# Optimization experiments

Measured on AMD Instinct MI355X. Metric: run time of the kernel, lower is better.

## Reference

```python
import jax, jax.numpy as jnp
import numpy as np

D_MODEL = 768
D_INNER = 1536      # expand*d_model
D_STATE = 128
NHEADS = 12         # d_inner // headdim
HEADDIM = 128
D_CONV = 4
CONV_DIM = D_INNER + 2 * D_STATE   # 1792 (ngroups=1)
D_IN_PROJ = 2 * D_INNER + 2 * D_STATE + NHEADS  # 3340


def setup_inputs() -> dict:
    key = jax.random.key(0)
    it = iter(jax.random.split(key, 24))
    def rn(shape, s):
        return jax.random.normal(next(it), shape, jnp.float32) * s
    inp = {}
    inp['x'] = jax.random.normal(next(it), (8, 12, 4096), jnp.float32)
    # conv stem
    inp['w1'] = rn((192, 12, 5), 0.2); inp['b1'] = jnp.zeros((192,))
    inp['bn1_g'] = jnp.ones((192,)); inp['bn1_b'] = jnp.zeros((192,)); inp['bn1_m'] = jnp.zeros((192,)); inp['bn1_v'] = jnp.ones((192,))
    inp['w2'] = rn((384, 192, 3), 0.05); inp['b2'] = jnp.zeros((384,))
    inp['bn2_g'] = jnp.ones((384,)); inp['bn2_b'] = jnp.zeros((384,)); inp['bn2_m'] = jnp.zeros((384,)); inp['bn2_v'] = jnp.ones((384,))
    inp['w3'] = rn((768, 384, 3), 0.05); inp['b3'] = jnp.zeros((768,))
    inp['bn3_g'] = jnp.ones((768,)); inp['bn3_b'] = jnp.zeros((768,)); inp['bn3_m'] = jnp.zeros((768,)); inp['bn3_v'] = jnp.ones((768,))
    # Mamba2 backbone
    inp['in_proj_w'] = rn((D_IN_PROJ, D_MODEL), 0.02)
    inp['conv_w'] = rn((CONV_DIM, D_CONV), 0.2)
    inp['conv_b'] = jnp.zeros((CONV_DIM,))
    inp['dt_bias'] = rn((NHEADS,), 0.5)
    inp['A_log'] = jnp.log(jax.random.uniform(next(it), (NHEADS,), minval=1.0, maxval=16.0))
    inp['D'] = jnp.ones((NHEADS,))
    inp['norm_w'] = jnp.ones((D_INNER,))
    inp['out_proj_w'] = rn((D_MODEL, D_INNER), 0.02)
    # classifier
    inp['fc1_w'] = rn((1024, 768), 0.02); inp['fc1_b'] = jnp.zeros((1024,))
    inp['bnc_g'] = jnp.ones((1024,)); inp['bnc_b'] = jnp.zeros((1024,)); inp['bnc_m'] = jnp.zeros((1024,)); inp['bnc_v'] = jnp.ones((1024,))
    inp['fc2_w'] = rn((27, 1024), 0.02); inp['fc2_b'] = jnp.zeros((27,))
    return inp


def _conv1d(x, w, b, stride, pad):
    y = jax.lax.conv_general_dilated(x, w, (stride,), [(pad, pad)], dimension_numbers=('NCH', 'OIH', 'NCH'))
    return y + b[None, :, None]


def _bn(x, g, b, m, v, eps=1e-5):
    sh = (1, -1, 1) if x.ndim == 3 else (1, -1)
    return (x - m.reshape(sh)) * jax.lax.rsqrt(v.reshape(sh) + eps) * g.reshape(sh) + b.reshape(sh)


def _forward(x, w1, b1, bn1_g, bn1_b, bn1_m, bn1_v, w2, b2, bn2_g, bn2_b, bn2_m, bn2_v,
             w3, b3, bn3_g, bn3_b, bn3_m, bn3_v, in_proj_w, conv_w, conv_b, dt_bias,
             A_log, D, norm_w, out_proj_w, fc1_w, fc1_b, bnc_g, bnc_b, bnc_m, bnc_v, fc2_w, fc2_b):
    gelu = lambda t: jax.nn.gelu(t, approximate=False)
    # conv stem (B, 12, 4096) -> (B, 768, 1024)
    h = _bn(gelu(_conv1d(x, w1, b1, 2, 2)), bn1_g, bn1_b, bn1_m, bn1_v)
    h = _bn(gelu(_conv1d(h, w2, b2, 2, 1)), bn2_g, bn2_b, bn2_m, bn2_v)
    h = _bn(gelu(_conv1d(h, w3, b3, 1, 1)), bn3_g, bn3_b, bn3_m, bn3_v)
    u = h.transpose(0, 2, 1)  # (B, L, 768)
    # Mamba2
    zxbcdt = u @ in_proj_w.T  # (B, L, 3340)
    z = zxbcdt[..., :D_INNER]
    xBC = zxbcdt[..., D_INNER:D_INNER + CONV_DIM]
    dt = jax.nn.softplus(zxbcdt[..., D_INNER + CONV_DIM:] + dt_bias)  # (B, L, H)
    # causal depthwise conv over time + silu
    xc = jax.lax.conv_general_dilated(xBC.transpose(0, 2, 1), conv_w[:, None, :], (1,), [(D_CONV - 1, 0)],
                                      dimension_numbers=('NCH', 'OIH', 'NCH'), feature_group_count=CONV_DIM)
    xBC = jax.nn.silu(xc + conv_b[None, :, None]).transpose(0, 2, 1)
    xs = xBC[..., :D_INNER]
    Bm = xBC[..., D_INNER:D_INNER + D_STATE]   # (B, L, N), ngroups=1
    Cm = xBC[..., D_INNER + D_STATE:]
    A = -jnp.exp(A_log)  # (H,)
    b_, l_ = xs.shape[0], xs.shape[1]
    xh = xs.reshape(b_, l_, NHEADS, HEADDIM)
    dA = jnp.exp(dt * A)  # (B, L, H)
    tm = lambda t: jnp.moveaxis(t, 1, 0)
    def step(state, inps):
        x_t, dA_t, dt_t, B_t, C_t = inps
        # state: (B, H, P, N)
        state = state * dA_t[..., None, None] + (dt_t[..., None] * x_t)[..., None] * B_t[:, None, None, :]
        y_t = jnp.einsum('bhpn,bn->bhp', state, C_t)
        return state, y_t
    state0 = jnp.zeros((b_, NHEADS, HEADDIM, D_STATE), xs.dtype)
    _, ys = jax.lax.scan(step, state0, (tm(xh), tm(dA), tm(dt), tm(Bm), tm(Cm)))
    y = jnp.moveaxis(ys, 0, 1) + D[None, None, :, None] * xh  # (B, L, H, P)
    y = y.reshape(b_, l_, D_INNER)
    # gated RMSNorm (norm_before_gate=False)
    y = y * jax.nn.silu(z)
    y = y * jax.lax.rsqrt(jnp.mean(y * y, axis=-1, keepdims=True) + 1e-5) * norm_w
    out = y @ out_proj_w.T  # (B, L, 768)
    rep = out.mean(axis=1)
    h1 = jax.nn.relu(_bn(rep @ fc1_w.T + fc1_b, bnc_g, bnc_b, bnc_m, bnc_v))
    return h1 @ fc2_w.T + fc2_b


def reference(x, w1, b1, bn1_g, bn1_b, bn1_m, bn1_v, w2, b2, bn2_g, bn2_b, bn2_m, bn2_v,
              w3, b3, bn3_g, bn3_b, bn3_m, bn3_v, in_proj_w, conv_w, conv_b, dt_bias,
              A_log, D, norm_w, out_proj_w, fc1_w, fc1_b, bnc_g, bnc_b, bnc_m, bnc_v, fc2_w, fc2_b):
    return _forward(x, w1, b1, bn1_g, bn1_b, bn1_m, bn1_v, w2, b2, bn2_g, bn2_b, bn2_m, bn2_v,
                    w3, b3, bn3_g, bn3_b, bn3_m, bn3_v, in_proj_w, conv_w, conv_b, dt_bias,
                    A_log, D, norm_w, out_proj_w, fc1_w, fc1_b, bnc_g, bnc_b, bnc_m, bnc_v, fc2_w, fc2_b)
```

## Files before the change

### kernel.cpp

```cpp
#include <hip/hip_runtime.h>
#include <math.h>

#define DEV __device__ __forceinline__

DEV float geluf(float x){ return 0.5f*x*(1.0f+erff(x*0.7071067811865476f)); }
DEV float siluf(float x){ return x/(1.0f+expf(-x)); }
DEV float softplusf(float x){ return fmaxf(x,0.0f)+log1pf(expf(-fabsf(x))); }
DEV unsigned short f2bf(float f){
  unsigned int u = __float_as_uint(f);
  unsigned int r = (u + 0x7fffu + ((u>>16)&1u)) >> 16;
  return (unsigned short)r;
}

typedef __attribute__((ext_vector_type(8))) short short8;
typedef __attribute__((ext_vector_type(4))) float f32x4;

__global__ void conv1_k(const float* __restrict__ x, const float* __restrict__ w,
                        const float* __restrict__ bias,
                        const float* __restrict__ g, const float* __restrict__ bb,
                        const float* __restrict__ m, const float* __restrict__ v,
                        float* __restrict__ out){
  int t  = blockIdx.x*256 + threadIdx.x;
  int og = blockIdx.y;
  int b  = blockIdx.z;
  const float* xb = x + (size_t)b*12*4096;
  float acc[8];
  #pragma unroll
  for(int oo=0;oo<8;++oo) acc[oo] = bias[og*8+oo];
  for(int i=0;i<12;++i){
    float xv[5];
    #pragma unroll
    for(int k=0;k<5;++k){
      int src = 2*t + k - 2;
      xv[k] = (src>=0 && src<4096) ? xb[i*4096+src] : 0.0f;
    }
    #pragma unroll
    for(int oo=0;oo<8;++oo){
      const float* wr = w + (size_t)(og*8+oo)*60 + i*5;
      #pragma unroll
      for(int k=0;k<5;++k) acc[oo] = fmaf(wr[k], xv[k], acc[oo]);
    }
  }
  #pragma unroll
  for(int oo=0;oo<8;++oo){
    int o = og*8+oo;
    float y = geluf(acc[oo]);
    float sc = g[o]*rsqrtf(v[o]+1e-5f);
    y = (y-m[o])*sc + bb[o];
    out[(size_t)b*192*2048 + (size_t)o*2048 + t] = y;
  }
}

__global__ void xpose1_k(const float* __restrict__ h1, unsigned short* __restrict__ T1){
  __shared__ float tile[32][33];
  int t0 = blockIdx.x*32, i0 = blockIdx.y*32, b = blockIdx.z;
  int c = threadIdx.x & 31, r4 = threadIdx.x >> 5;
  const float* src = h1 + (size_t)b*393216;
  #pragma unroll
  for(int i=0;i<4;++i){ int r = r4 + i*8; tile[r][c] = src[(size_t)(i0+r)*2048 + t0 + c]; }
  __syncthreads();
  unsigned short* dst = T1 + (size_t)b*2048*192;
  #pragma unroll
  for(int i=0;i<4;++i){ int r = r4 + i*8;
    dst[(size_t)(t0+r)*192 + i0 + c] = f2bf(tile[c][r]);
  }
}

__global__ void wprep_k(const float* __restrict__ ipw, const float* __restrict__ w2,
                        const float* __restrict__ w3, unsigned short* __restrict__ Wb,
                        unsigned short* __restrict__ w2r, unsigned short* __restrict__ w3r){
  int gid = blockIdx.x*256 + threadIdx.x;
  if(gid < 2555904){
    Wb[gid] = f2bf(ipw[gid]);
  } else if(gid < 2555904+221184){
    int g2 = gid - 2555904;
    int o = g2 / 576, rem = g2 - o*576, k = rem / 192, i = rem - k*192;
    w2r[g2] = f2bf(w2[(size_t)o*576 + i*3 + k]);
  } else if(gid < 2555904+221184+884736){
    int g3 = gid - 2555904 - 221184;
    int o = g3 / 1152, rem = g3 - o*1152, k = rem / 384, i = rem - k*384;
    w3r[g3] = f2bf(w3[(size_t)o*1152 + i*3 + k]);
  }
}

__global__ __launch_bounds__(256) void conv2_mfma(const unsigned short* __restrict__ A,
                                                  const unsigned short* __restrict__ W,
                                                  const float* __restrict__ bias,
                                                  const float* __restrict__ g, const float* __restrict__ bb,
                                                  const float* __restrict__ bm, const float* __restrict__ bv,
                                                  unsigned short* __restrict__ outb){
  __shared__ unsigned short As[4096], Bs[4096];
  const int tid = threadIdx.x;
  const int lane = tid & 63, wave = tid >> 6;
  const int wm = wave & 1, wn = wave >> 1;
  const int m0 = blockIdx.y*128, n0 = blockIdx.x*128;
  const int bidx = m0 >> 10, tloc = m0 & 1023;
  f32x4 acc[4][4];
  #pragma unroll
  for(int i=0;i<4;++i)
    #pragma unroll
    for(int j=0;j<4;++j) acc[i][j] = (f32x4){0.f,0.f,0.f,0.f};
  const int u0 = tid, u1 = tid + 256;
  const int r0 = u0>>2, kl0 = (u0&3) ^ ((r0>>1)&3);
  const int r1 = u1>>2, kl1 = (u1&3) ^ ((r1>>1)&3);
  const int kg = lane>>4, ml = lane&15;
  const short8 z8 = {0,0,0,0,0,0,0,0};
  for(int kb=0; kb<3; ++kb){
    int ta = 2*(tloc + r0) + kb - 1;
    int tb = 2*(tloc + r1) + kb - 1;
    bool va = (ta>=0) && (ta<2048);
    bool vb = (tb>=0) && (tb<2048);
    const unsigned short* pa = A + ((size_t)bidx*2048 + ta)*192;
    const unsigned short* pb = A + ((size_t)bidx*2048 + tb)*192;
    for(int c0=0; c0<192; c0+=32){
      int k0 = kb*192 + c0;
      short8 a0 = va ? *reinterpret_cast<const short8*>(pa + c0 + kl0*8) : z8;
      short8 a1 = vb ? *reinterpret_cast<const short8*>(pb + c0 + kl1*8) : z8;
      short8 b0 = *reinterpret_cast<const short8*>(W + (size_t)(n0+r0)*576 + k0 + kl0*8);
      short8 b1 = *reinterpret_cast<const short8*>(W + (size_t)(n0+r1)*576 + k0 + kl1*8);
      __syncthreads();
      *reinterpret_cast<short8*>(As + u0*8) = a0;
      *reinterpret_cast<short8*>(As + u1*8) = a1;
      *reinterpret_cast<short8*>(Bs + u0*8) = b0;
      *reinterpret_cast<short8*>(Bs + u1*8) = b1;
      __syncthreads();
      short8 af[4], bfr[4];
      #pragma unroll
      for(int f=0;f<4;++f){
        int row = wm*64 + f*16 + ml;
        int un  = row*4 + (kg ^ ((row>>1)&3));
        af[f] = *reinterpret_cast<const short8*>(As + un*8);
        int rowb = wn*64 + f*16 + ml;
        int ub   = rowb*4 + (kg ^ ((rowb>>1)&3));
        bfr[f] = *reinterpret_cast<const short8*>(Bs + ub*8);
      }
      #pragma unroll
      for(int i=0;i<4;++i)
        #pragma unroll
        for(int j=0;j<4;++j)
          acc[i][j] = __builtin_amdgcn_mfma_f32_16x16x32_bf16(af[i], bfr[j], acc[i][j], 0, 0, 0);
    }
  }
  #pragma unroll
  for(int i=0;i<4;++i){
    int rb = m0 + wm*64 + i*16 + kg*4;
    #pragma unroll
    for(int j=0;j<4;++j){
      int col = n0 + wn*64 + j*16 + ml;
      float sc = g[col]*rsqrtf(bv[col]+1e-5f);
      float mm = bm[col], bbv = bb[col], bi = bias[col];
      #pragma unroll
      for(int r=0;r<4;++r){
        float yv = geluf(acc[i][j][r] + bi);
        yv = (yv - mm)*sc + bbv;
        outb[(size_t)(rb+r)*384 + col] = f2bf(yv);
      }
    }
  }
}

__global__ __launch_bounds__(256) void conv3_mfma(const unsigned short* __restrict__ A,
                                                  const unsigned short* __restrict__ W,
                                                  const float* __restrict__ bias,
                                                  const float* __restrict__ g, const float* __restrict__ bb,
                                                  const float* __restrict__ bm, const float* __restrict__ bv,
                                                  unsigned short* __restrict__ outb,
                                                  float* __restrict__ outf){
  __shared__ unsigned short As[4096], Bs[4096];
  const int tid = threadIdx.x;
  const int lane = tid & 63, wave = tid >> 6;
  const int wm = wave & 1, wn = wave >> 1;
  const int m0 = blockIdx.y*128, n0 = blockIdx.x*128;
  const int bidx = m0 >> 10, tloc = m0 & 1023;
  f32x4 acc[4][4];
  #pragma unroll
  for(int i=0;i<4;++i)
    #pragma unroll
    for(int j=0;j<4;++j) acc[i][j] = (f32x4){0.f,0.f,0.f,0.f};
  const int u0 = tid, u1 = tid + 256;
  const int r0 = u0>>2, kl0 = (u0&3) ^ ((r0>>1)&3);
  const int r1 = u1>>2, kl1 = (u1&3) ^ ((r1>>1)&3);
  const int kg = lane>>4, ml = lane&15;
  const short8 z8 = {0,0,0,0,0,0,0,0};
  for(int kb=0; kb<3; ++kb){
    int ta = tloc + r0 + kb - 1;
    int tb = tloc + r1 + kb - 1;
    bool va = (ta>=0) && (ta<1024);
    bool vb = (tb>=0) && (tb<1024);
    const unsigned short* pa = A + ((size_t)bidx*1024 + ta)*384;
    const unsigned short* pb = A + ((size_t)bidx*1024 + tb)*384;
    for(int c0=0; c0<384; c0+=32){
      int k0 = kb*384 + c0;
      short8 a0 = va ? *reinterpret_cast<const short8*>(pa + c0 + kl0*8) : z8;
      short8 a1 = vb ? *reinterpret_cast<const short8*>(pb + c0 + kl1*8) : z8;
      short8 b0 = *reinterpret_cast<const short8*>(W + (size_t)(n0+r0)*1152 + k0 + kl0*8);
      short8 b1 = *reinterpret_cast<const short8*>(W + (size_t)(n0+r1)*1152 + k0 + kl1*8);
      __syncthreads();
      *reinterpret_cast<short8*>(As + u0*8) = a0;
      *reinterpret_cast<short8*>(As + u1*8) = a1;
      *reinterpret_cast<short8*>(Bs + u0*8) = b0;
      *reinterpret_cast<short8*>(Bs + u1*8) = b1;
      __syncthreads();
      short8 af[4], bfr[4];
      #pragma unroll
      for(int f=0;f<4;++f){
        int row = wm*64 + f*16 + ml;
        int un  = row*4 + (kg ^ ((row>>1)&3));
        af[f] = *reinterpret_cast<const short8*>(As + un*8);
        int rowb = wn*64 + f*16 + ml;
        int ub   = rowb*4 + (kg ^ ((rowb>>1)&3));
        bfr[f] = *reinterpret_cast<const short8*>(Bs + ub*8);
      }
      #pragma unroll
      for(int i=0;i<4;++i)
        #pragma unroll
        for(int j=0;j<4;++j)
          acc[i][j] = __builtin_amdgcn_mfma_f32_16x16x32_bf16(af[i], bfr[j], acc[i][j], 0, 0, 0);
    }
  }
  #pragma unroll
  for(int i=0;i<4;++i){
    int rb = m0 + wm*64 + i*16 + kg*4;
    #pragma unroll
    for(int j=0;j<4;++j){
      int col = n0 + wn*64 + j*16 + ml;
      float sc = g[col]*rsqrtf(bv[col]+1e-5f);
      float mm = bm[col], bbv = bb[col], bi = bias[col];
      #pragma unroll
      for(int r=0;r<4;++r){
        float yv = geluf(acc[i][j][r] + bi);
        yv = (yv - mm)*sc + bbv;
        outb[(size_t)(rb+r)*768 + col] = f2bf(yv);
        outf[(size_t)(rb+r)*768 + col] = yv;
      }
    }
  }
}

__global__ __launch_bounds__(256) void inproj_mfma(const unsigned short* __restrict__ A,
                                                   const unsigned short* __restrict__ B,
                                                   float* __restrict__ Z, float* __restrict__ XB){
  __shared__ unsigned short As[4096], Bs[4096];
  const int tid = threadIdx.x;
  const int lane = tid & 63, wave = tid >> 6;
  const int wm = wave & 1, wn = wave >> 1;
  const int m0 = blockIdx.y*128, n0 = blockIdx.x*128;
  f32x4 acc[4][4];
  #pragma unroll
  for(int i=0;i<4;++i)
    #pragma unroll
    for(int j=0;j<4;++j) acc[i][j] = (f32x4){0.f,0.f,0.f,0.f};
  const int u0 = tid, u1 = tid + 256;
  const int r0 = u0>>2, kl0 = (u0&3) ^ ((r0>>1)&3);
  const int r1 = u1>>2, kl1 = (u1&3) ^ ((r1>>1)&3);
  const int kg = lane>>4, ml = lane&15;
  for(int k0=0;k0<768;k0+=32){
    short8 a0 = *reinterpret_cast<const short8*>(A + (size_t)(m0+r0)*768 + k0 + kl0*8);
    short8 a1 = *reinterpret_cast<const short8*>(A + (size_t)(m0+r1)*768 + k0 + kl1*8);
    short8 b0 = *reinterpret_cast<const short8*>(B + (size_t)(n0+r0)*768 + k0 + kl0*8);
    short8 b1 = *reinterpret_cast<const short8*>(B + (size_t)(n0+r1)*768 + k0 + kl1*8);
    __syncthreads();
    *reinterpret_cast<short8*>(As + u0*8) = a0;
    *reinterpret_cast<short8*>(As + u1*8) = a1;
    *reinterpret_cast<short8*>(Bs + u0*8) = b0;
    *reinterpret_cast<short8*>(Bs + u1*8) = b1;
    __syncthreads();
    short8 af[4], bfr[4];
    #pragma unroll
    for(int f=0;f<4;++f){
      int row = wm*64 + f*16 + ml;
      int un  = row*4 + (kg ^ ((row>>1)&3));
      af[f] = *reinterpret_cast<const short8*>(As + un*8);
      int rowb = wn*64 + f*16 + ml;
      int ub   = rowb*4 + (kg ^ ((rowb>>1)&3));
      bfr[f] = *reinterpret_cast<const short8*>(Bs + ub*8);
    }
    #pragma unroll
    for(int i=0;i<4;++i)
      #pragma unroll
      for(int j=0;j<4;++j)
        acc[i][j] = __builtin_amdgcn_mfma_f32_16x16x32_bf16(af[i], bfr[j], acc[i][j], 0, 0, 0);
  }
  float* op; int cb; int stride;
  if(n0 < 1536){ op = Z;  cb = n0;        stride = 1536; }
  else         { op = XB; cb = n0 - 1536; stride = 1792; }
  #pragma unroll
  for(int i=0;i<4;++i){
    int rb = m0 + wm*64 + i*16 + kg*4;
    #pragma unroll
    for(int j=0;j<4;++j){
      int col = cb + wn*64 + j*16 + ml;
      #pragma unroll
      for(int r=0;r<4;++r)
        op[(size_t)(rb+r)*stride + col] = acc[i][j][r];
    }
  }
}

__global__ __launch_bounds__(256) void dtgemm2_k(const float* __restrict__ h3f, const float* __restrict__ W,
                                                 const float* __restrict__ dt_bias, const float* __restrict__ A_log,
                                                 float* __restrict__ dt, float* __restrict__ dA){
  __shared__ float Ws[12][768];
  __shared__ float Ah[12], Bh[12];
  int tid = threadIdx.x;
  for(int idx=tid; idx<9216; idx+=256){
    int hh = idx/768, k = idx - hh*768;
    Ws[hh][k] = W[(size_t)(3328+hh)*768 + k];
  }
  if(tid<12){ Ah[tid] = -expf(A_log[tid]); Bh[tid] = dt_bias[tid]; }
  __syncthreads();
  int wave = tid>>6, lane = tid&63;
  int m = blockIdx.x*4 + wave;
  const float* xr = h3f + (size_t)m*768;
  float xv[12];
  #pragma unroll
  for(int q=0;q<12;++q) xv[q] = xr[q*64+lane];
  float res[12];
  #pragma unroll
  for(int h=0;h<12;++h){
    float acc = 0.f;
    #pragma unroll
    for(int q=0;q<12;++q) acc = fmaf(xv[q], Ws[h][q*64+lane], acc);
    #pragma unroll
    for(int off=32;off;off>>=1) acc += __shfl_xor(acc, off);
    res[h] = acc;
  }
  if(lane==0){
    #pragma unroll
    for(int h=0;h<12;++h){
      float sp = softplusf(res[h] + Bh[h]);
      dt[(size_t)m*12+h] = sp;
      dA[(size_t)m*12+h] = expf(sp*Ah[h]);
    }
  }
}

__global__ void dwconv_k(const float* __restrict__ XB, const float* __restrict__ cw,
                         const float* __restrict__ cb, float* __restrict__ xs,
                         float* __restrict__ Bo, float* __restrict__ Co){
  int gid = blockIdx.x*256 + threadIdx.x;
  int c4 = gid % 448;
  int m = gid / 448;
  int t = m & 1023;
  int c = c4*4;
  float wA[4][4];
  #pragma unroll
  for(int i=0;i<4;++i)
    *reinterpret_cast<float4*>(wA[i]) = *reinterpret_cast<const float4*>(&cw[(c+i)*4]);
  float4 bi = *reinterpret_cast<const float4*>(&cb[c]);
  float av[4] = {bi.x, bi.y, bi.z, bi.w};
  #pragma unroll
  for(int j=0;j<4;++j){
    int tt = t - 3 + j;
    if(tt >= 0){
      float4 xv = *reinterpret_cast<const float4*>(&XB[(size_t)(m-3+j)*1792 + c]);
      av[0] = fmaf(wA[0][j], xv.x, av[0]);
      av[1] = fmaf(wA[1][j], xv.y, av[1]);
      av[2] = fmaf(wA[2][j], xv.z, av[2]);
      av[3] = fmaf(wA[3][j], xv.w, av[3]);
    }
  }
  float4 res = make_float4(siluf(av[0]), siluf(av[1]), siluf(av[2]), siluf(av[3]));
  if(c4 < 384)      *reinterpret_cast<float4*>(&xs[(size_t)m*1536 + c])        = res;
  else if(c4 < 416) *reinterpret_cast<float4*>(&Bo[(size_t)m*128 + (c-1536)])  = res;
  else              *reinterpret_cast<float4*>(&Co[(size_t)m*128 + (c-1664)])  = res;
}

__global__ void cumda_k(const float* __restrict__ dA, float* __restrict__ cda){
  __shared__ float ld[1024];
  int bh = blockIdx.x; int b = bh/12, hh = bh - b*12;
  int tid = threadIdx.x;
  for(int i=tid;i<1024;i+=128) ld[i] = dA[((size_t)b*1024 + i)*12 + hh];
  __syncthreads();
  for(int c=0;c<8;++c){
    int base = c*128;
    for(int off=1;off<128;off<<=1){
      float v = ld[base+tid];
      if(tid>=off) v *= ld[base+tid-off];
      __syncthreads();
      ld[base+tid] = v;
      __syncthreads();
    }
  }
  for(int i=tid;i<1024;i+=128) cda[(size_t)bh*1024 + i] = ld[i];
}

#define SSTEP(E, BQE, CQE) \
  s[0][jj*4+E] = fmaf(s[0][jj*4+E], dav, c0*BQE); y0 = fmaf(s[0][jj*4+E], CQE, y0); \
  s[1][jj*4+E] = fmaf(s[1][jj*4+E], dav, c1*BQE); y1 = fmaf(s[1][jj*4+E], CQE, y1); \
  s[2][jj*4+E] = fmaf(s[2][jj*4+E], dav, c2*BQE); y2 = fmaf(s[2][jj*4+E], CQE, y2); \
  s[3][jj*4+E] = fmaf(s[3][jj*4+E], dav, c3*BQE); y3 = fmaf(s[3][jj*4+E], CQE, y3);

__global__ __launch_bounds__(128) void scan_chunk_k(float* __restrict__ xs,
    const float* __restrict__ Bm, const float* __restrict__ Cm,
    const float* __restrict__ dtb, const float* __restrict__ dAb,
    const float* __restrict__ Dv, float* __restrict__ sfin){
  const int c = blockIdx.x, h = blockIdx.y, b = blockIdx.z;
  const int tid = threadIdx.x;
  const int ng = tid & 3, pg = tid >> 2;
  __shared__ float lx[16][128], lB[16][144], lC[16][144], ly[16][128];
  __shared__ float ldt[16], lda_[16];
  float s[4][32];
  #pragma unroll
  for(int i=0;i<4;++i)
    #pragma unroll
    for(int j=0;j<32;++j) s[i][j]=0.f;
  const float Dh = Dv[h];
  const size_t mb = (size_t)b*1024 + (size_t)c*128;
  for(int t0=0;t0<128;t0+=16){
    for(int idx=tid; idx<2048; idx+=128){
      int tl = idx>>7, cc = idx&127;
      lx[tl][cc] = xs[(mb+t0+tl)*1536 + h*128 + cc];
      int slot = (cc>>5)*36 + (cc&31);
      lB[tl][slot] = Bm[(mb+t0+tl)*128 + cc];
      lC[tl][slot] = Cm[(mb+t0+tl)*128 + cc];
    }
    if(tid<16){
      ldt[tid]  = dtb[(mb+t0+tid)*12 + h];
      lda_[tid] = dAb[(mb+t0+tid)*12 + h];
    }
    __syncthreads();
    for(int tl=0; tl<16; ++tl){
      float dtv = ldt[tl], dav = lda_[tl];
      float4 xq = *reinterpret_cast<const float4*>(&lx[tl][pg*4]);
      float c0 = dtv*xq.x, c1 = dtv*xq.y, c2 = dtv*xq.z, c3 = dtv*xq.w;
      float y0=0.f,y1=0.f,y2=0.f,y3=0.f;
      #pragma unroll
      for(int jj=0;jj<8;++jj){
        float4 bq = *reinterpret_cast<const float4*>(&lB[tl][ng*36+jj*4]);
        float4 cq = *reinterpret_cast<const float4*>(&lC[tl][ng*36+jj*4]);
        SSTEP(0, bq.x, cq.x)
        SSTEP(1, bq.y, cq.y)
        SSTEP(2, bq.z, cq.z)
        SSTEP(3, bq.w, cq.w)
      }
      y0 += __shfl_xor(y0,1); y0 += __shfl_xor(y0,2);
      y1 += __shfl_xor(y1,1); y1 += __shfl_xor(y1,2);
      y2 += __shfl_xor(y2,1); y2 += __shfl_xor(y2,2);
      y3 += __shfl_xor(y3,1); y3 += __shfl_xor(y3,2);
      if(ng==0) *reinterpret_cast<float4*>(&ly[tl][pg*4]) = make_float4(y0,y1,y2,y3);
    }
    __syncthreads();
    for(int idx=tid; idx<2048; idx+=128){
      int tl = idx>>7, cc = idx&127;
      xs[(mb+t0+tl)*1536 + h*128 + cc] = ly[tl][cc] + Dh*lx[tl][cc];
    }
    __syncthreads();
  }
  float* dst = sfin + ((size_t)(b*12+h)*8 + c)*16384;
  #pragma unroll
  for(int jj=0;jj<8;++jj)
    #pragma unroll
    for(int e=0;e<4;++e){
      int n = ng*32 + jj*4 + e;
      *reinterpret_cast<float4*>(&dst[(size_t)n*128 + pg*4]) =
        make_float4(s[0][jj*4+e], s[1][jj*4+e], s[2][jj*4+e], s[3][jj*4+e]);
    }
}

__global__ __launch_bounds__(256) void correct_k(const float* __restrict__ Cm,
    const float* __restrict__ cumdA, const float* __restrict__ sfin,
    float* __restrict__ ys){
  const int c = blockIdx.x + 1, h = blockIdx.y, b = blockIdx.z;
  const int tid = threadIdx.x;
  const size_t bh = (size_t)b*12 + h;
  __shared__ float Sl[16][128];
  __shared__ float Cl[16][132];
  __shared__ float cumP[128];
  __shared__ float coefs[8];
  if(tid==0){
    float cf = 1.f;
    for(int cp=c-1; cp>=0; --cp){
      coefs[cp] = cf;
      cf *= cumdA[bh*1024 + (size_t)cp*128 + 127];
    }
  }
  if(tid<128) cumP[tid] = cumdA[bh*1024 + (size_t)c*128 + tid];
  __syncthreads();
  const int tp = tid>>4, tt = tid&15;
  float acc[8][8];
  #pragma unroll
  for(int i=0;i<8;++i)
    #pragma unroll
    for(int j=0;j<8;++j) acc[i][j]=0.f;
  const size_t mb = (size_t)b*1024 + (size_t)c*128;
  for(int n0=0;n0<128;n0+=16){
    {
      int kk = tid>>4, po = tid&15;
      float4 v0 = {0,0,0,0}, v1 = {0,0,0,0};
      for(int cp=0; cp<c; ++cp){
        const float* sp = sfin + ((bh*8 + cp)*16384) + (size_t)(n0+kk)*128 + po*8;
        float4 a0 = *reinterpret_cast<const float4*>(sp);
        float4 a1 = *reinterpret_cast<const float4*>(sp+4);
        float cf = coefs[cp];
        v0.x = fmaf(cf,a0.x,v0.x); v0.y = fmaf(cf,a0.y,v0.y);
        v0.z = fmaf(cf,a0.z,v0.z); v0.w = fmaf(cf,a0.w,v0.w);
        v1.x = fmaf(cf,a1.x,v1.x); v1.y = fmaf(cf,a1.y,v1.y);
        v1.z = fmaf(cf,a1.z,v1.z); v1.w = fmaf(cf,a1.w,v1.w);
      }
      *reinterpret_cast<float4*>(&Sl[kk][po*8])   = v0;
      *reinterpret_cast<float4*>(&Sl[kk][po*8+4]) = v1;
    }
    #pragma unroll
    for(int e=0;e<8;++e){
      int idx = tid*8 + e; int tl = idx>>4, kk = idx&15;
      Cl[kk][tl] = Cm[(mb + tl)*128 + n0 + kk];
    }
    __syncthreads();
    #pragma unroll
    for(int kk=0;kk<16;++kk){
      float4 sa = *reinterpret_cast<const float4*>(&Sl[kk][tp*8]);
      float4 sb = *reinterpret_cast<const float4*>(&Sl[kk][tp*8+4]);
      float4 ca = *reinterpret_cast<const float4*>(&Cl[kk][tt*8]);
      float4 cb = *reinterpret_cast<const float4*>(&Cl[kk][tt*8+4]);
      float sv[8] = {sa.x,sa.y,sa.z,sa.w,sb.x,sb.y,sb.z,sb.w};
      float cv[8] = {ca.x,ca.y,ca.z,ca.w,cb.x,cb.y,cb.z,cb.w};
      #pragma unroll
      for(int i=0;i<8;++i)
        #pragma unroll
        for(int j=0;j<8;++j) acc[i][j] = fmaf(sv[i], cv[j], acc[i][j]);
    }
    __syncthreads();
  }
  #pragma unroll
  for(int j=0;j<8;++j){
    int tl = tt*8 + j;
    float cp = cumP[tl];
    float* yp = ys + (mb + tl)*1536 + h*128 + tp*8;
    float4 y0 = *reinterpret_cast<float4*>(yp);
    float4 y1 = *reinterpret_cast<float4*>(yp+4);
    y0.x += cp*acc[0][j]; y0.y += cp*acc[1][j]; y0.z += cp*acc[2][j]; y0.w += cp*acc[3][j];
    y1.x += cp*acc[4][j]; y1.y += cp*acc[5][j]; y1.z += cp*acc[6][j]; y1.w += cp*acc[7][j];
    *reinterpret_cast<float4*>(yp)   = y0;
    *reinterpret_cast<float4*>(yp+4) = y1;
  }
}

__global__ void gate_k(const float* __restrict__ ys, const float* __restrict__ Z,
                       const float* __restrict__ nw, float* __restrict__ ybp){
  int m = blockIdx.x;
  int b = m >> 10, t = m & 1023;
  int tid = threadIdx.x;
  float gvals[6];
  float ss = 0.0f;
  #pragma unroll
  for(int r=0;r<6;++r){
    int c = r*256 + tid;
    float yv = ys[(size_t)m*1536 + c];
    float zv = Z[(size_t)m*1536 + c];
    float gv = yv * siluf(zv);
    gvals[r] = gv;
    ss = fmaf(gv, gv, ss);
  }
  #pragma unroll
  for(int off=32;off;off>>=1) ss += __shfl_xor(ss, off);
  __shared__ float red[4];
  if((tid&63)==0) red[tid>>6] = ss;
  __syncthreads();
  float tot = red[0]+red[1]+red[2]+red[3];
  float scale = rsqrtf(tot*(1.0f/1536.0f) + 1e-5f);
  float* dst = ybp + ((size_t)(t&7)*8 + b)*1536;
  #pragma unroll
  for(int r=0;r<6;++r){
    int c = r*256 + tid;
    atomicAdd(&dst[c], gvals[r]*scale*nw[c]);
  }
}

__global__ void ybm_k(const float* __restrict__ ybp, float* __restrict__ ybm){
  int idx = blockIdx.x*256 + threadIdx.x;
  float s = 0.0f;
  #pragma unroll
  for(int p=0;p<8;++p) s += ybp[(size_t)p*12288 + idx];
  ybm[idx] = s * (1.0f/1024.0f);
}

__global__ void rep_k(const float* __restrict__ ybm, const float* __restrict__ W,
                      float* __restrict__ rep){
  int wid  = (blockIdx.x<<2) + (threadIdx.x>>6);
  int lane = threadIdx.x & 63;
  int b = wid / 768, o = wid % 768;
  const float* xr = ybm + (size_t)b*1536;
  const float* wr = W + (size_t)o*1536;
  float acc = 0.0f;
  for(int c=lane;c<1536;c+=64) acc = fmaf(xr[c], wr[c], acc);
  #pragma unroll
  for(int off=32;off;off>>=1) acc += __shfl_xor(acc, off);
  if(lane==0) rep[wid] = acc;
}

__global__ void fc1_k(const float* __restrict__ rep, const float* __restrict__ W,
                      const float* __restrict__ bias, const float* __restrict__ g,
                      const float* __restrict__ bb, const float* __restrict__ m,
                      const float* __restrict__ v, float* __restrict__ out){
  int wid  = (blockIdx.x<<2) + (threadIdx.x>>6);
  int lane = threadIdx.x & 63;
  int b = wid >> 10, o = wid & 1023;
  const float* xr = rep + (size_t)b*768;
  const float* wr = W + (size_t)o*768;
  float acc = 0.0f;
  for(int c=lane;c<768;c+=64) acc = fmaf(xr[c], wr[c], acc);
  #pragma unroll
  for(int off=32;off;off>>=1) acc += __shfl_xor(acc, off);
  if(lane==0){
    float val = acc + bias[o];
    float sc = g[o]*rsqrtf(v[o]+1e-5f);
    val = (val - m[o])*sc + bb[o];
    out[wid] = fmaxf(val, 0.0f);
  }
}

__global__ void fc2_k(const float* __restrict__ h1, const float* __restrict__ W,
                      const float* __restrict__ bias, float* __restrict__ out){
  int wid  = (blockIdx.x<<2) + (threadIdx.x>>6);
  int lane = threadIdx.x & 63;
  int b = wid / 27, o = wid % 27;
  const float* xr = h1 + (size_t)b*1024;
  const float* wr = W + (size_t)o*1024;
  float acc = 0.0f;
  for(int c=lane;c<1024;c+=64) acc = fmaf(xr[c], wr[c], acc);
  #pragma unroll
  for(int off=32;off;off>>=1) acc += __shfl_xor(acc, off);
  if(lane==0) out[wid] = acc + bias[o];
}

#define OFF_H1     0u
#define OFF_T1     3145728u
#define OFF_T2     4718592u
#define OFF_H3T    6291456u
#define OFF_WB     9437184u
#define OFF_W2R    10715136u
#define OFF_W3R    10825728u
#define OFF_Z      12582912u
#define OFF_XB     25165824u
#define OFF_XS     39944192u
#define OFF_H3F    39944192u
#define OFF_B      52527104u
#define OFF_C      53575680u
#define OFF_DT     54624256u
#define OFF_DA     54722560u
#define OFF_SLOT98K 54820864u
#define OFF_YBM    54919168u
#define OFF_REP    54931456u
#define OFF_FC1    54937600u
#define OFF_SFIN   0u

extern "C" void kernel_launch(void* const* d_in, const int* in_sizes, int n_in,
                              void* d_out, int out_size, void* d_ws, size_t ws_size,
                              hipStream_t stream){
  const float* x       = (const float*)d_in[0];
  const float* w1      = (const float*)d_in[1];
  const float* b1      = (const float*)d_in[2];
  const float* bn1g    = (const float*)d_in[3];
  const float* bn1b    = (const float*)d_in[4];
  const float* bn1m    = (const float*)d_in[5];
  const float* bn1v    = (const float*)d_in[6];
  const float* w2      = (const float*)d_in[7];
  const float* b2      = (const float*)d_in[8];
  const float* bn2g    = (const float*)d_in[9];
  const float* bn2b    = (const float*)d_in[10];
  const float* bn2m    = (const float*)d_in[11];
  const float* bn2v    = (const float*)d_in[12];
  const float* w3      = (const float*)d_in[13];
  const float* b3      = (const float*)d_in[14];
  const float* bn3g    = (const float*)d_in[15];
  const float* bn3b    = (const float*)d_in[16];
  const float* bn3m    = (const float*)d_in[17];
  const float* bn3v    = (const float*)d_in[18];
  const float* ipw     = (const float*)d_in[19];
  const float* convw   = (const float*)d_in[20];
  const float* convb   = (const float*)d_in[21];
  const float* dtbias  = (const float*)d_in[22];
  const float* Alog    = (const float*)d_in[23];
  const float* Dvec    = (const float*)d_in[24];
  const float* normw   = (const float*)d_in[25];
  const float* opw     = (const float*)d_in[26];
  const float* fc1w    = (const float*)d_in[27];
  const float* fc1b    = (const float*)d_in[28];
  const float* bncg    = (const float*)d_in[29];
  const float* bncb    = (const float*)d_in[30];
  const float* bncm    = (const float*)d_in[31];
  const float* bncv    = (const float*)d_in[32];
  const float* fc2w    = (const float*)d_in[33];
  const float* fc2b    = (const float*)d_in[34];

  float* ws   = (float*)d_ws;
  float* h1   = ws + OFF_H1;
  unsigned short* T1  = (unsigned short*)(ws + OFF_T1);
  unsigned short* T2  = (unsigned short*)(ws + OFF_T2);
  unsigned short* h3t = (unsigned short*)(ws + OFF_H3T);
  unsigned short* Wb  = (unsigned short*)(ws + OFF_WB);
  unsigned short* w2r = (unsigned short*)(ws + OFF_W2R);
  unsigned short* w3r = (unsigned short*)(ws + OFF_W3R);
  float* Zb   = ws + OFF_Z;
  float* XBb  = ws + OFF_XB;
  float* xsb  = ws + OFF_XS;
  float* h3f  = ws + OFF_H3F;
  float* Bb   = ws + OFF_B;
  float* Cb   = ws + OFF_C;
  float* dtb  = ws + OFF_DT;
  float* dAb  = ws + OFF_DA;
  float* slot = ws + OFF_SLOT98K;
  float* ybm  = ws + OFF_YBM;
  float* rep  = ws + OFF_REP;
  float* f1b  = ws + OFF_FC1;
  float* sfin = ws + OFF_SFIN;
  float* outp = (float*)d_out;

  conv1_k<<<dim3(8,24,8),  256, 0, stream>>>(x, w1, b1, bn1g, bn1b, bn1m, bn1v, h1);
  xpose1_k<<<dim3(64,6,8), 256, 0, stream>>>(h1, T1);
  wprep_k<<<14304, 256, 0, stream>>>(ipw, w2, w3, Wb, w2r, w3r);
  conv2_mfma<<<dim3(3,64), 256, 0, stream>>>(T1, w2r, b2, bn2g, bn2b, bn2m, bn2v, T2);
  conv3_mfma<<<dim3(6,64), 256, 0, stream>>>(T2, w3r, b3, bn3g, bn3b, bn3m, bn3v, h3t, h3f);
  dtgemm2_k<<<2048, 256, 0, stream>>>(h3f, ipw, dtbias, Alog, dtb, dAb);
  inproj_mfma<<<dim3(26,64), 256, 0, stream>>>(h3t, Wb, Zb, XBb);
  dwconv_k<<<14336, 256, 0, stream>>>(XBb, convw, convb, xsb, Bb, Cb);
  cumda_k<<<96, 128, 0, stream>>>(dAb, slot);
  scan_chunk_k<<<dim3(8,12,8), 128, 0, stream>>>(xsb, Bb, Cb, dtb, dAb, Dvec, sfin);
  correct_k<<<dim3(7,12,8), 256, 0, stream>>>(Cb, slot, sfin, xsb);
  hipMemsetAsync(slot, 0, 98304*sizeof(float), stream);
  gate_k<<<8192, 256, 0, stream>>>(xsb, Zb, normw, slot);
  ybm_k<<<48, 256, 0, stream>>>(slot, ybm);
  rep_k<<<1536, 256, 0, stream>>>(ybm, opw, rep);
  fc1_k<<<2048, 256, 0, stream>>>(rep, fc1w, fc1b, bncg, bncb, bncm, bncv, f1b);
  fc2_k<<<54, 256, 0, stream>>>(f1b, fc2w, fc2b, outp);
}
```

Before: 751.1 us.

## Replace sequential intra-chunk scan with SSD matrix form on bf16 MFMA

The per-chunk sequential recurrence kernel is replaced by a chunked SSD formulation. Each chunk computes C·Bᵀ, applies a causal mask with exp(cumsum log-decay) weights, multiplies by dt·x, and forms the chunk-end state, all as bf16 MFMA matmuls in swizzled LDS. The cumulative decay is now a log-space prefix sum, and B/C are stored as bf16 to halve their traffic. The goal is to turn a latency-bound serial loop into matrix-core work. The cost is reduced precision from bf16 x/B/C, partly offset by a hi/lo split of the decay matrix.

```diff
diff --git a/kernel.cpp b/kernel.cpp
--- a/kernel.cpp
+++ b/kernel.cpp
@@ -11,6 +11,7 @@
   unsigned int r = (u + 0x7fffu + ((u>>16)&1u)) >> 16;
   return (unsigned short)r;
 }
+DEV float bf2f(unsigned short u){ return __uint_as_float(((unsigned int)u)<<16); }
 
 typedef __attribute__((ext_vector_type(8))) short short8;
 typedef __attribute__((ext_vector_type(4))) float f32x4;
@@ -298,16 +299,16 @@
 }
 
 __global__ __launch_bounds__(256) void dtgemm2_k(const float* __restrict__ h3f, const float* __restrict__ W,
-                                                 const float* __restrict__ dt_bias, const float* __restrict__ A_log,
-                                                 float* __restrict__ dt, float* __restrict__ dA){
+                                                 const float* __restrict__ dt_bias,
+                                                 float* __restrict__ dt){
   __shared__ float Ws[12][768];
-  __shared__ float Ah[12], Bh[12];
+  __shared__ float Bh[12];
   int tid = threadIdx.x;
   for(int idx=tid; idx<9216; idx+=256){
     int hh = idx/768, k = idx - hh*768;
     Ws[hh][k] = W[(size_t)(3328+hh)*768 + k];
   }
-  if(tid<12){ Ah[tid] = -expf(A_log[tid]); Bh[tid] = dt_bias[tid]; }
+  if(tid<12){ Bh[tid] = dt_bias[tid]; }
   __syncthreads();
   int wave = tid>>6, lane = tid&63;
   int m = blockIdx.x*4 + wave;
@@ -328,16 +329,14 @@
   if(lane==0){
     #pragma unroll
     for(int h=0;h<12;++h){
-      float sp = softplusf(res[h] + Bh[h]);
-      dt[(size_t)m*12+h] = sp;
-      dA[(size_t)m*12+h] = expf(sp*Ah[h]);
+      dt[(size_t)m*12+h] = softplusf(res[h] + Bh[h]);
     }
   }
 }
 
 __global__ void dwconv_k(const float* __restrict__ XB, const float* __restrict__ cw,
                          const float* __restrict__ cb, float* __restrict__ xs,
-                         float* __restrict__ Bo, float* __restrict__ Co){
+                         unsigned short* __restrict__ Bo, unsigned short* __restrict__ Co){
   int gid = blockIdx.x*256 + threadIdx.x;
   int c4 = gid % 448;
   int m = gid / 448;
@@ -360,105 +359,210 @@
       av[3] = fmaf(wA[3][j], xv.w, av[3]);
     }
   }
-  float4 res = make_float4(siluf(av[0]), siluf(av[1]), siluf(av[2]), siluf(av[3]));
-  if(c4 < 384)      *reinterpret_cast<float4*>(&xs[(size_t)m*1536 + c])        = res;
-  else if(c4 < 416) *reinterpret_cast<float4*>(&Bo[(size_t)m*128 + (c-1536)])  = res;
-  else              *reinterpret_cast<float4*>(&Co[(size_t)m*128 + (c-1664)])  = res;
-}
-
-__global__ void cumda_k(const float* __restrict__ dA, float* __restrict__ cda){
+  float r0 = siluf(av[0]), r1 = siluf(av[1]), r2 = siluf(av[2]), r3 = siluf(av[3]);
+  if(c4 < 384){
+    *reinterpret_cast<float4*>(&xs[(size_t)m*1536 + c]) = make_float4(r0,r1,r2,r3);
+  } else {
+    unsigned long long pk = (unsigned long long)f2bf(r0)
+                          | ((unsigned long long)f2bf(r1) << 16)
+                          | ((unsigned long long)f2bf(r2) << 32)
+                          | ((unsigned long long)f2bf(r3) << 48);
+    if(c4 < 416) *reinterpret_cast<unsigned long long*>(&Bo[(size_t)m*128 + (c-1536)]) = pk;
+    else         *reinterpret_cast<unsigned long long*>(&Co[(size_t)m*128 + (c-1664)]) = pk;
+  }
+}
+
+__global__ void cumda_k(const float* __restrict__ dtb, const float* __restrict__ Alog,
+                        float* __restrict__ cda, float* __restrict__ lab){
   __shared__ float ld[1024];
   int bh = blockIdx.x; int b = bh/12, hh = bh - b*12;
   int tid = threadIdx.x;
-  for(int i=tid;i<1024;i+=128) ld[i] = dA[((size_t)b*1024 + i)*12 + hh];
+  float Ah = -expf(Alog[hh]);
+  for(int i=tid;i<1024;i+=128) ld[i] = dtb[((size_t)b*1024 + i)*12 + hh] * Ah;
   __syncthreads();
   for(int c=0;c<8;++c){
     int base = c*128;
     for(int off=1;off<128;off<<=1){
       float v = ld[base+tid];
-      if(tid>=off) v *= ld[base+tid-off];
+      if(tid>=off) v += ld[base+tid-off];
       __syncthreads();
       ld[base+tid] = v;
       __syncthreads();
     }
   }
-  for(int i=tid;i<1024;i+=128) cda[(size_t)bh*1024 + i] = ld[i];
-}
-
-#define SSTEP(E, BQE, CQE) \
-  s[0][jj*4+E] = fmaf(s[0][jj*4+E], dav, c0*BQE); y0 = fmaf(s[0][jj*4+E], CQE, y0); \
-  s[1][jj*4+E] = fmaf(s[1][jj*4+E], dav, c1*BQE); y1 = fmaf(s[1][jj*4+E], CQE, y1); \
-  s[2][jj*4+E] = fmaf(s[2][jj*4+E], dav, c2*BQE); y2 = fmaf(s[2][jj*4+E], CQE, y2); \
-  s[3][jj*4+E] = fmaf(s[3][jj*4+E], dav, c3*BQE); y3 = fmaf(s[3][jj*4+E], CQE, y3);
-
-__global__ __launch_bounds__(128) void scan_chunk_k(float* __restrict__ xs,
-    const float* __restrict__ Bm, const float* __restrict__ Cm,
-    const float* __restrict__ dtb, const float* __restrict__ dAb,
+  for(int i=tid;i<1024;i+=128){
+    lab[(size_t)bh*1024 + i] = ld[i];
+    cda[(size_t)bh*1024 + i] = expf(ld[i]);
+  }
+}
+
+__global__ __launch_bounds__(256) void ssd_k(float* __restrict__ xs,
+    const unsigned short* __restrict__ Bm, const unsigned short* __restrict__ Cm,
+    const float* __restrict__ dtb, const float* __restrict__ lab,
     const float* __restrict__ Dv, float* __restrict__ sfin){
   const int c = blockIdx.x, h = blockIdx.y, b = blockIdx.z;
   const int tid = threadIdx.x;
-  const int ng = tid & 3, pg = tid >> 2;
-  __shared__ float lx[16][128], lB[16][144], lC[16][144], ly[16][128];
-  __shared__ float ldt[16], lda_[16];
-  float s[4][32];
+  const int lane = tid & 63, wave = tid >> 6;
+  const int wm = wave & 1, wn = wave >> 1;
+  const int kg = lane>>4, ml = lane&15;
+  __shared__ unsigned short Cb[16384], Bb[16384], Xt[16384];
+  __shared__ float la[128], dtc[128];
+  const size_t mb = (size_t)b*1024 + (size_t)c*128;
+  const size_t bh = (size_t)b*12 + h;
+  if(tid < 128){
+    la[tid]  = lab[bh*1024 + (size_t)c*128 + tid];
+    dtc[tid] = dtb[(mb+tid)*12 + h];
+  }
+  for(int g = tid; g < 2048; g += 256){
+    int r = g >> 4, oct = g & 15;
+    int ck = oct >> 2, o = oct & 3;
+    int u = ck*4096 + (r*4 + (o ^ ((r>>1)&3)))*8;
+    *reinterpret_cast<short8*>(Cb + u) = *reinterpret_cast<const short8*>(Cm + (mb+r)*128 + ck*32 + o*8);
+    *reinterpret_cast<short8*>(Bb + u) = *reinterpret_cast<const short8*>(Bm + (mb+r)*128 + ck*32 + o*8);
+  }
+  __syncthreads();
+  for(int a = tid; a < 4096; a += 256){
+    int j = a >> 5, pq = a & 31;
+    float4 xv = *reinterpret_cast<const float4*>(&xs[(mb+j)*1536 + h*128 + pq*4]);
+    float dj = dtc[j];
+    int ck = j>>5, o = (j>>3)&3, e = j&7;
+    float vv[4] = {xv.x, xv.y, xv.z, xv.w};
+    #pragma unroll
+    for(int q=0;q<4;++q){
+      int p = pq*4+q;
+      Xt[ck*4096 + (p*4 + (o ^ ((p>>1)&3)))*8 + e] = f2bf(vv[q]*dj);
+    }
+  }
+  __syncthreads();
+  f32x4 accM[4][4];
   #pragma unroll
   for(int i=0;i<4;++i)
     #pragma unroll
-    for(int j=0;j<32;++j) s[i][j]=0.f;
+    for(int j=0;j<4;++j) accM[i][j] = (f32x4){0.f,0.f,0.f,0.f};
+  for(int ck=0;ck<4;++ck){
+    short8 af[4], bfr[4];
+    #pragma unroll
+    for(int f=0;f<4;++f){
+      int row = wm*64 + f*16 + ml;
+      af[f] = *reinterpret_cast<const short8*>(Cb + ck*4096 + (row*4 + (kg ^ ((row>>1)&3)))*8);
+      int rowb = wn*64 + f*16 + ml;
+      bfr[f] = *reinterpret_cast<const short8*>(Bb + ck*4096 + (rowb*4 + (kg ^ ((rowb>>1)&3)))*8);
+    }
+    #pragma unroll
+    for(int i=0;i<4;++i)
+      #pragma unroll
+      for(int j=0;j<4;++j)
+        accM[i][j] = __builtin_amdgcn_mfma_f32_16x16x32_bf16(af[i], bfr[j], accM[i][j], 0, 0, 0);
+  }
+  __syncthreads();
+  #pragma unroll
+  for(int fj=0;fj<4;++fj){
+    int j = wn*64 + fj*16 + ml;
+    float laj = la[j];
+    int jck = j>>5, jo = (j>>3)&3, je = j&7;
+    #pragma unroll
+    for(int fi=0;fi<4;++fi){
+      #pragma unroll
+      for(int r=0;r<4;++r){
+        int i = wm*64 + fi*16 + kg*4 + r;
+        float v = (j <= i) ? accM[fi][fj][r] * expf(la[i]-laj) : 0.f;
+        unsigned short hi = f2bf(v);
+        unsigned short lo = f2bf(v - bf2f(hi));
+        int idx = jck*4096 + (i*4 + (jo ^ ((i>>1)&3)))*8 + je;
+        Cb[idx] = hi; Bb[idx] = lo;
+      }
+    }
+  }
+  __syncthreads();
+  f32x4 accY[4][4];
+  #pragma unroll
+  for(int i=0;i<4;++i)
+    #pragma unroll
+    for(int j=0;j<4;++j) accY[i][j] = (f32x4){0.f,0.f,0.f,0.f};
+  for(int ck=0;ck<4;++ck){
+    short8 aH[4], aL[4], bX[4];
+    #pragma unroll
+    for(int f=0;f<4;++f){
+      int row = wm*64 + f*16 + ml;
+      int ua = ck*4096 + (row*4 + (kg ^ ((row>>1)&3)))*8;
+      aH[f] = *reinterpret_cast<const short8*>(Cb + ua);
+      aL[f] = *reinterpret_cast<const short8*>(Bb + ua);
+      int rowp = wn*64 + f*16 + ml;
+      bX[f] = *reinterpret_cast<const short8*>(Xt + ck*4096 + (rowp*4 + (kg ^ ((rowp>>1)&3)))*8);
+    }
+    #pragma unroll
+    for(int i=0;i<4;++i)
+      #pragma unroll
+      for(int j=0;j<4;++j){
+        accY[i][j] = __builtin_amdgcn_mfma_f32_16x16x32_bf16(aH[i], bX[j], accY[i][j], 0, 0, 0);
+        accY[i][j] = __builtin_amdgcn_mfma_f32_16x16x32_bf16(aL[i], bX[j], accY[i][j], 0, 0, 0);
+      }
+  }
   const float Dh = Dv[h];
-  const size_t mb = (size_t)b*1024 + (size_t)c*128;
-  for(int t0=0;t0<128;t0+=16){
-    for(int idx=tid; idx<2048; idx+=128){
-      int tl = idx>>7, cc = idx&127;
-      lx[tl][cc] = xs[(mb+t0+tl)*1536 + h*128 + cc];
-      int slot = (cc>>5)*36 + (cc&31);
-      lB[tl][slot] = Bm[(mb+t0+tl)*128 + cc];
-      lC[tl][slot] = Cm[(mb+t0+tl)*128 + cc];
-    }
-    if(tid<16){
-      ldt[tid]  = dtb[(mb+t0+tid)*12 + h];
-      lda_[tid] = dAb[(mb+t0+tid)*12 + h];
-    }
-    __syncthreads();
-    for(int tl=0; tl<16; ++tl){
-      float dtv = ldt[tl], dav = lda_[tl];
-      float4 xq = *reinterpret_cast<const float4*>(&lx[tl][pg*4]);
-      float c0 = dtv*xq.x, c1 = dtv*xq.y, c2 = dtv*xq.z, c3 = dtv*xq.w;
-      float y0=0.f,y1=0.f,y2=0.f,y3=0.f;
-      #pragma unroll
-      for(int jj=0;jj<8;++jj){
-        float4 bq = *reinterpret_cast<const float4*>(&lB[tl][ng*36+jj*4]);
-        float4 cq = *reinterpret_cast<const float4*>(&lC[tl][ng*36+jj*4]);
-        SSTEP(0, bq.x, cq.x)
-        SSTEP(1, bq.y, cq.y)
-        SSTEP(2, bq.z, cq.z)
-        SSTEP(3, bq.w, cq.w)
+  #pragma unroll
+  for(int fi=0;fi<4;++fi){
+    #pragma unroll
+    for(int fj=0;fj<4;++fj){
+      int p = wn*64 + fj*16 + ml;
+      #pragma unroll
+      for(int r=0;r<4;++r){
+        int t = wm*64 + fi*16 + kg*4 + r;
+        float* ap = &xs[(mb+t)*1536 + h*128 + p];
+        float old = *ap;
+        *ap = accY[fi][fj][r] + Dh*old;
       }
-      y0 += __shfl_xor(y0,1); y0 += __shfl_xor(y0,2);
-      y1 += __shfl_xor(y1,1); y1 += __shfl_xor(y1,2);
-      y2 += __shfl_xor(y2,1); y2 += __shfl_xor(y2,2);
-      y3 += __shfl_xor(y3,1); y3 += __shfl_xor(y3,2);
-      if(ng==0) *reinterpret_cast<float4*>(&ly[tl][pg*4]) = make_float4(y0,y1,y2,y3);
-    }
-    __syncthreads();
-    for(int idx=tid; idx<2048; idx+=128){
-      int tl = idx>>7, cc = idx&127;
-      xs[(mb+t0+tl)*1536 + h*128 + cc] = ly[tl][cc] + Dh*lx[tl][cc];
-    }
-    __syncthreads();
-  }
-  float* dst = sfin + ((size_t)(b*12+h)*8 + c)*16384;
-  #pragma unroll
-  for(int jj=0;jj<8;++jj)
-    #pragma unroll
-    for(int e=0;e<4;++e){
-      int n = ng*32 + jj*4 + e;
-      *reinterpret_cast<float4*>(&dst[(size_t)n*128 + pg*4]) =
-        make_float4(s[0][jj*4+e], s[1][jj*4+e], s[2][jj*4+e], s[3][jj*4+e]);
-    }
-}
-
-__global__ __launch_bounds__(256) void correct_k(const float* __restrict__ Cm,
+    }
+  }
+  __syncthreads();
+  float laF = la[127];
+  for(int a = tid; a < 2048; a += 256){
+    int j = a >> 4, noct = a & 15;
+    float wj = expf(laF - la[j]);
+    int ck = j>>5, o = (j>>3)&3, e = j&7;
+    #pragma unroll
+    for(int q=0;q<8;++q){
+      int n = noct*8+q;
+      float v = bf2f(Bm[(mb+j)*128 + n]) * wj;
+      Cb[ck*4096 + (n*4 + (o ^ ((n>>1)&3)))*8 + e] = f2bf(v);
+    }
+  }
+  __syncthreads();
+  f32x4 accS[4][4];
+  #pragma unroll
+  for(int i=0;i<4;++i)
+    #pragma unroll
+    for(int j=0;j<4;++j) accS[i][j] = (f32x4){0.f,0.f,0.f,0.f};
+  for(int ck=0;ck<4;++ck){
+    short8 aW[4], bX[4];
+    #pragma unroll
+    for(int f=0;f<4;++f){
+      int row = wm*64 + f*16 + ml;
+      aW[f] = *reinterpret_cast<const short8*>(Cb + ck*4096 + (row*4 + (kg ^ ((row>>1)&3)))*8);
+      int rowp = wn*64 + f*16 + ml;
+      bX[f] = *reinterpret_cast<const short8*>(Xt + ck*4096 + (rowp*4 + (kg ^ ((rowp>>1)&3)))*8);
+    }
+    #pragma unroll
+    for(int i=0;i<4;++i)
+      #pragma unroll
+      for(int j=0;j<4;++j)
+        accS[i][j] = __builtin_amdgcn_mfma_f32_16x16x32_bf16(aW[i], bX[j], accS[i][j], 0, 0, 0);
+  }
+  float* dst = sfin + (bh*8 + (size_t)c)*16384;
+  #pragma unroll
+  for(int fi=0;fi<4;++fi){
+    #pragma unroll
+    for(int fj=0;fj<4;++fj){
+      int p = wn*64 + fj*16 + ml;
+      #pragma unroll
+      for(int r=0;r<4;++r){
+        int n = wm*64 + fi*16 + kg*4 + r;
+        dst[(size_t)n*128 + p] = accS[fi][fj][r];
+      }
+    }
+  }
+}
+
+__global__ __launch_bounds__(256) void correct_k(const unsigned short* __restrict__ Cm,
     const float* __restrict__ cumdA, const float* __restrict__ sfin,
     float* __restrict__ ys){
   const int c = blockIdx.x + 1, h = blockIdx.y, b = blockIdx.z;
@@ -504,7 +608,7 @@
     #pragma unroll
     for(int e=0;e<8;++e){
       int idx = tid*8 + e; int tl = idx>>4, kk = idx&15;
-      Cl[kk][tl] = Cm[(mb + tl)*128 + n0 + kk];
+      Cl[kk][tl] = bf2f(Cm[(mb + tl)*128 + n0 + kk]);
     }
     __syncthreads();
     #pragma unroll
@@ -696,10 +800,10 @@
   float* XBb  = ws + OFF_XB;
   float* xsb  = ws + OFF_XS;
   float* h3f  = ws + OFF_H3F;
-  float* Bb   = ws + OFF_B;
-  float* Cb   = ws + OFF_C;
+  unsigned short* Bo = (unsigned short*)(ws + OFF_B);
+  unsigned short* Co = (unsigned short*)(ws + OFF_C);
   float* dtb  = ws + OFF_DT;
-  float* dAb  = ws + OFF_DA;
+  float* lab  = ws + OFF_DA;
   float* slot = ws + OFF_SLOT98K;
   float* ybm  = ws + OFF_YBM;
   float* rep  = ws + OFF_REP;
@@ -712,12 +816,12 @@
   wprep_k<<<14304, 256, 0, stream>>>(ipw, w2, w3, Wb, w2r, w3r);
   conv2_mfma<<<dim3(3,64), 256, 0, stream>>>(T1, w2r, b2, bn2g, bn2b, bn2m, bn2v, T2);
   conv3_mfma<<<dim3(6,64), 256, 0, stream>>>(T2, w3r, b3, bn3g, bn3b, bn3m, bn3v, h3t, h3f);
-  dtgemm2_k<<<2048, 256, 0, stream>>>(h3f, ipw, dtbias, Alog, dtb, dAb);
+  dtgemm2_k<<<2048, 256, 0, stream>>>(h3f, ipw, dtbias, dtb);
   inproj_mfma<<<dim3(26,64), 256, 0, stream>>>(h3t, Wb, Zb, XBb);
-  dwconv_k<<<14336, 256, 0, stream>>>(XBb, convw, convb, xsb, Bb, Cb);
-  cumda_k<<<96, 128, 0, stream>>>(dAb, slot);
-  scan_chunk_k<<<dim3(8,12,8), 128, 0, stream>>>(xsb, Bb, Cb, dtb, dAb, Dvec, sfin);
-  correct_k<<<dim3(7,12,8), 256, 0, stream>>>(Cb, slot, sfin, xsb);
+  dwconv_k<<<14336, 256, 0, stream>>>(XBb, convw, convb, xsb, Bo, Co);
+  cumda_k<<<96, 128, 0, stream>>>(dtb, Alog, slot, lab);
+  ssd_k<<<dim3(8,12,8), 256, 0, stream>>>(xsb, Bo, Co, dtb, lab, Dvec, sfin);
+  correct_k<<<dim3(7,12,8), 256, 0, stream>>>(Co, slot, sfin, xsb);
   hipMemsetAsync(slot, 0, 98304*sizeof(float), stream);
   gate_k<<<8192, 256, 0, stream>>>(xsb, Zb, normw, slot);
   ybm_k<<<48, 256, 0, stream>>>(slot, ybm);
```

Result: faster. 649.2 us (-13.6%).
